# Performance work log

Hardware: AMD Instinct MI355X
Metric: run time of the kernel (lower is better)

Reference implementation:

```python
import jax, jax.numpy as jnp
import numpy as np

N_CIR, N_DIS, D, H = 585, 88, 128, 8
E_CC, E_DD = 20000, 3000
EPS = 1e-16


def _gcn(x, src, dst, ew, W, b, N):
    # PyG GCNConv: add self-loops (weight 1), symmetric normalization, x @ W, scatter-add, + bias
    loop = jnp.arange(N)
    s = jnp.concatenate([src, loop])
    d = jnp.concatenate([dst, loop])
    w = jnp.concatenate([ew, jnp.ones((N,), ew.dtype)])
    deg = jax.ops.segment_sum(w, d, num_segments=N)
    dinv = jnp.where(deg > 0, jax.lax.rsqrt(deg), 0.0)
    norm = dinv[s] * w * dinv[d]                      # [E+N]
    h = x @ W                                         # [N,D]
    out = jax.ops.segment_sum(h[s] * norm[:, None], d, num_segments=N)
    return out + b


def _gat(x, src, dst, ea, W, a_src, a_dst, a_edge, We, b, N):
    # PyG GATConv(heads=H, concat=False, edge_dim=1): self-loops with mean edge_attr fill,
    # leaky_relu attention logits, segment softmax over destination, mean over heads, + bias
    loop = jnp.arange(N)
    s = jnp.concatenate([src, loop])
    d = jnp.concatenate([dst, loop])
    ea = jnp.concatenate([ea, jnp.broadcast_to(ea.mean(0, keepdims=True), (N, ea.shape[1]))], 0)
    h = (x @ W).reshape(N, H, D)                      # [N,H,D]
    e = (ea @ We).reshape(-1, H, D)                   # [E+N,H,D]
    alpha = (h * a_src).sum(-1)[s] + (h * a_dst).sum(-1)[d] + (e * a_edge).sum(-1)
    alpha = jax.nn.leaky_relu(alpha, 0.2)             # [E+N,H]
    amax = jax.ops.segment_max(alpha, d, num_segments=N)
    ex = jnp.exp(alpha - amax[d])
    den = jax.ops.segment_sum(ex, d, num_segments=N)
    alpha = ex / (den[d] + EPS)
    out = jax.ops.segment_sum(h[s] * alpha[:, :, None], d, num_segments=N)  # [N,H,D]
    return out.mean(1) + b


def _branch(x, edges, mat, gw1, gb1, aw, asrc, adst, aedge, awe, ab, gw2, gb2, N):
    src, dst = edges[0], edges[1]
    ew = mat[src, dst]                                # gather edge weights from dense matrix
    f1 = jax.nn.relu(_gcn(x, src, dst, ew, gw1, gb1, N))
    att = jax.nn.relu(_gat(f1, src, dst, ew[:, None], aw, asrc, adst, aedge, awe, ab, N))
    f2 = jax.nn.relu(_gcn(att, src, dst, ew, gw2, gb2, N))
    return f1, f2


def _cnn(f1, f2, Wk, b):
    # Conv2d(2,256,(128,1)) over [1,2,128,N] == per-node GEMM over (2,128) then view/transpose
    Xv = jnp.stack([f1.T, f2.T])                      # [2,D,N]
    return jnp.einsum('ock,ckn->no', Wk[..., 0], Xv) + b  # [N,256]


def setup_inputs():
    ks = jax.random.split(jax.random.key(0), 24)
    rn = lambda i, sh, s=1.0: jax.random.normal(ks[i], sh, jnp.float32) * s
    w = 0.08  # ~glorot scale for fan-in 128
    return {
        'x_cir': rn(0, (N_CIR, D)),
        'x_dis': rn(1, (N_DIS, D)),
        'cc_matrix': jax.random.uniform(ks[2], (N_CIR, N_CIR), jnp.float32),
        'dd_matrix': jax.random.uniform(ks[3], (N_DIS, N_DIS), jnp.float32),
        'gcn_c1_w': rn(4, (D, D), w), 'gcn_c1_b': jnp.zeros((D,), jnp.float32),
        'gat_c_w': rn(5, (D, H * D), w), 'gat_c_asrc': rn(6, (H, D), w),
        'gat_c_adst': rn(7, (H, D), w), 'gat_c_aedge': rn(8, (H, D), w),
        'gat_c_we': rn(9, (1, H * D), w), 'gat_c_b': jnp.zeros((D,), jnp.float32),
        'gcn_c2_w': rn(10, (D, D), w), 'gcn_c2_b': jnp.zeros((D,), jnp.float32),
        'gcn_d1_w': rn(11, (D, D), w), 'gcn_d1_b': jnp.zeros((D,), jnp.float32),
        'gat_d_w': rn(12, (D, H * D), w), 'gat_d_asrc': rn(13, (H, D), w),
        'gat_d_adst': rn(14, (H, D), w), 'gat_d_aedge': rn(15, (H, D), w),
        'gat_d_we': rn(16, (1, H * D), w), 'gat_d_b': jnp.zeros((D,), jnp.float32),
        'gcn_d2_w': rn(17, (D, D), w), 'gcn_d2_b': jnp.zeros((D,), jnp.float32),
        'conv_c_w': rn(18, (256, 2, D, 1), w), 'conv_c_b': jnp.zeros((256,), jnp.float32),
        'conv_d_w': rn(19, (256, 2, D, 1), w), 'conv_d_b': jnp.zeros((256,), jnp.float32),
        'cc_edges': jax.random.randint(ks[20], (2, E_CC), 0, N_CIR),
        'dd_edges': jax.random.randint(ks[21], (2, E_DD), 0, N_DIS),
    }


def reference(x_cir, x_dis, cc_matrix, dd_matrix,
              gcn_c1_w, gcn_c1_b, gat_c_w, gat_c_asrc, gat_c_adst, gat_c_aedge, gat_c_we, gat_c_b,
              gcn_c2_w, gcn_c2_b,
              gcn_d1_w, gcn_d1_b, gat_d_w, gat_d_asrc, gat_d_adst, gat_d_aedge, gat_d_we, gat_d_b,
              gcn_d2_w, gcn_d2_b,
              conv_c_w, conv_c_b, conv_d_w, conv_d_b,
              cc_edges, dd_edges):
    c1, c2 = _branch(x_cir, cc_edges, cc_matrix, gcn_c1_w, gcn_c1_b, gat_c_w, gat_c_asrc,
                     gat_c_adst, gat_c_aedge, gat_c_we, gat_c_b, gcn_c2_w, gcn_c2_b, N_CIR)
    d1, d2 = _branch(x_dis, dd_edges, dd_matrix, gcn_d1_w, gcn_d1_b, gat_d_w, gat_d_asrc,
                     gat_d_adst, gat_d_aedge, gat_d_we, gat_d_b, gcn_d2_w, gcn_d2_b, N_DIS)
    cir_fea = _cnn(c1, c2, conv_c_w, conv_c_b)        # [585,256]
    dis_fea = _cnn(d1, d2, conv_d_w, conv_d_b)        # [88,256]
    return cir_fea @ dis_fea.T, cir_fea, dis_fea
```

## Files before the change

kernel.cpp:

```cpp
#include <hip/hip_runtime.h>

constexpr int NCIR = 585;
constexpr int NDIS = 88;
constexpr int NT   = NCIR + NDIS;
constexpr int DIM  = 128;
constexpr int NH   = 8;
constexpr int ECC  = 20000;
constexpr int EDD  = 3000;
constexpr int ET   = ECC + EDD;
constexpr int CO   = 256;
constexpr int F1C  = (NCIR + 3) / 4;
constexpr int F1D  = (NDIS + 3) / 4;
constexpr int NG   = F1C + F1D;
constexpr int CH   = 64;
constexpr int GBK  = (ET + 255) / 256;
constexpr int GEMB = (NT + 1) / 2;

struct P {
  const float *x_c, *x_d, *mat_c, *mat_d;
  const float *g1w_c, *g1b_c, *aw_c, *as_c, *ad_c, *ae_c, *we_c, *ab_c, *g2w_c, *g2b_c;
  const float *g1w_d, *g1b_d, *aw_d, *as_d, *ad_d, *ae_d, *we_d, *ab_d, *g2w_d, *g2b_d;
  const float *cw_c, *cb_c, *cw_d, *cb_d;
  const int *csrc, *cdst, *dsrc, *ddst;
  float *ew, *dinv, *easum, *wedot, *hs, *hd, *h, *f1, *hg, *fill_w, *psc, *psd, *wdeg;
  int *cnt, *cursor, *rowptr, *fill_s;
  float *out_score, *out_cir, *out_dis;
};

__global__ __launch_bounds__(256) void k_gg(P p){
  __shared__ float r0[256], r1[256];
  int b = blockIdx.x, t = threadIdx.x;
  if (b < GBK){
    int e = b * 256 + t;
    float wc = 0.0f, wdv = 0.0f;
    if (e < ET){
      float w; int d;
      if (e < ECC){
        int s = p.csrc[e]; d = p.cdst[e];
        w = p.mat_c[s * NCIR + d]; wc = w;
      } else {
        int el = e - ECC;
        int s = p.dsrc[el]; d = NCIR + p.ddst[el];
        w = p.mat_d[s * NDIS + (d - NCIR)]; wdv = w;
      }
      p.ew[e] = w;
      atomicAdd(&p.wdeg[d], w);
      atomicAdd(&p.cnt[d], 1);
    }
    r0[t] = wc; r1[t] = wdv;
    __syncthreads();
    for (int st = 128; st; st >>= 1){
      if (t < st){ r0[t] += r0[t + st]; r1[t] += r1[t + st]; }
      __syncthreads();
    }
    if (t == 0){ p.psc[b] = r0[0]; p.psd[b] = r1[0]; }
  } else {
    float* a_sh = r0;
    int ub = (b - GBK) * 2;
    int n = t >> 7, k = t & 127;
    int u = ub + n;
    bool ok = u < NT;
    if (ok){
      int br = u >= NCIR;
      a_sh[n * DIM + k] = br ? p.x_d[(u - NCIR) * DIM + k] : p.x_c[u * DIM + k];
    }
    __syncthreads();
    if (ok){
      const float* W = (u >= NCIR) ? p.g1w_d : p.g1w_c;
      float acc = 0.0f;
      #pragma unroll 8
      for (int c = 0; c < DIM; ++c) acc += a_sh[n * DIM + c] * W[c * DIM + k];
      p.h[u * DIM + k] = acc;
    }
  }
}

__global__ __launch_bounds__(1024) void k_scan(P p){
  __shared__ int sd[1024];
  int t = threadIdx.x;
  int v0 = (t < NT) ? p.cnt[t] : 0;
  sd[t] = v0;
  __syncthreads();
  for (int off = 1; off < 1024; off <<= 1){
    int v = (t >= off) ? sd[t - off] : 0;
    __syncthreads();
    sd[t] += v;
    __syncthreads();
  }
  if (t < NT){
    p.rowptr[t + 1] = sd[t];
    p.cursor[t]     = sd[t] - v0;
    p.dinv[t] = rsqrtf(1.0f + p.wdeg[t]);
  }
  if (t == 0) p.rowptr[0] = 0;
  int wv = t >> 6, lane = t & 63;
  if (wv < 2){
    const float* ps = wv ? p.psd : p.psc;
    float v = ps[lane] + (lane + 64 < GBK ? ps[lane + 64] : 0.0f);
    #pragma unroll
    for (int off = 32; off; off >>= 1) v += __shfl_down(v, off, 64);
    if (lane == 0) p.easum[wv] = v / (wv ? (float)EDD : (float)ECC);
  }
  {
    int hh = wv & 7;
    const float* We = (wv >= 8) ? p.we_d : p.we_c;
    const float* Ae = (wv >= 8) ? p.ae_d : p.ae_c;
    float v = We[hh * DIM + lane] * Ae[hh * DIM + lane]
            + We[hh * DIM + 64 + lane] * Ae[hh * DIM + 64 + lane];
    #pragma unroll
    for (int off = 32; off; off >>= 1) v += __shfl_down(v, off, 64);
    if (lane == 0) p.wedot[wv] = v;
  }
}

__global__ __launch_bounds__(256) void k_fill(P p){
  int e = blockIdx.x * 256 + threadIdx.x;
  if (e >= ET) return;
  int s, d;
  if (e < ECC){ s = p.csrc[e]; d = p.cdst[e]; }
  else { int el = e - ECC; s = NCIR + p.dsrc[el]; d = NCIR + p.ddst[el]; }
  int pos = atomicAdd(&p.cursor[d], 1);
  p.fill_s[pos] = s;
  p.fill_w[pos] = p.ew[e];
}

__global__ __launch_bounds__(128) void k_agg1(P p){
  int d = blockIdx.x, k = threadIdx.x;
  int br = d >= NCIR;
  const float* B1 = br ? p.g1b_d : p.g1b_c;
  float dv = p.dinv[d];
  float acc = B1[k] + p.h[d * DIM + k] * dv * dv;
  int beg = p.rowptr[d], end = p.rowptr[d + 1];
  for (int j = beg; j < end; ++j){
    int s = p.fill_s[j];
    acc += p.h[s * DIM + k] * (p.dinv[s] * p.fill_w[j] * dv);
  }
  p.f1[d * DIM + k] = acc;
}

__global__ __launch_bounds__(256) void k_proj(P p){
  __shared__ float a_sh[4][DIM];
  __shared__ float wred[4][8];
  int b = blockIdx.x, t = threadIdx.x;
  int ng = b >> 2, ct = b & 3;
  int base, count, br;
  if (ng < F1C){ base = ng * 4; count = min(4, NCIR - base); br = 0; }
  else { base = NCIR + (ng - F1C) * 4; count = 4; br = 1; }
  for (int i = 0; i < 2; ++i){
    int idx = t + i * 256, n = idx >> 7, c = idx & 127;
    a_sh[n][c] = (n < count) ? fmaxf(p.f1[(base + n) * DIM + c], 0.0f) : 0.0f;
  }
  __syncthreads();
  const float* W = (br ? p.aw_d : p.aw_c) + ct * 256 + t;
  float acc[4] = {0.f, 0.f, 0.f, 0.f};
  #pragma unroll 4
  for (int c = 0; c < DIM; ++c){
    float w = W[c * 1024];
    acc[0] += a_sh[0][c] * w; acc[1] += a_sh[1][c] * w;
    acc[2] += a_sh[2][c] * w; acc[3] += a_sh[3][c] * w;
  }
  int col = ct * 256 + t;
  for (int n = 0; n < count; ++n)
    p.hg[(size_t)(base + n) * 1024 + col] = acc[n];
  const float* As = br ? p.as_d : p.as_c;
  const float* Ad = br ? p.ad_d : p.ad_c;
  float av = As[col], dw = Ad[col];
  int w = t >> 6;
  #pragma unroll
  for (int n = 0; n < 4; ++n){
    float sdot = acc[n] * av, ddot = acc[n] * dw;
    #pragma unroll
    for (int off = 32; off; off >>= 1){
      sdot += __shfl_down(sdot, off, 64);
      ddot += __shfl_down(ddot, off, 64);
    }
    if ((t & 63) == 0){ wred[w][n * 2] = sdot; wred[w][n * 2 + 1] = ddot; }
  }
  __syncthreads();
  if (t < 16){
    int g = t >> 3, v = t & 7, n = v >> 1, isd = v & 1;
    if (n < count){
      float sum = wred[g * 2][v] + wred[g * 2 + 1][v];
      float* dst = isd ? p.hd : p.hs;
      dst[(base + n) * NH + ct * 2 + g] = sum;
    }
  }
}

__global__ __launch_bounds__(256) void k_att(P p){
  __shared__ float den_sh[NH], hd_sh[NH], inv_sh[NH], wself_sh[NH];
  __shared__ float alpha_sh[CH * NH];
  __shared__ int   s_sh[CH];
  __shared__ float a2[2][DIM];
  __shared__ float attv[DIM];
  __shared__ float part[2][DIM];
  int d = blockIdx.x, t = threadIdx.x;
  int g = t >> 7, k = t & 127;
  int br = d >= NCIR;
  const float* wd = p.wedot + br * NH;
  if (t < NH){ den_sh[t] = 0.0f; hd_sh[t] = p.hd[d * NH + t]; }
  __syncthreads();
  int beg = p.rowptr[d], end = p.rowptr[d + 1];
  int deg = end - beg;
  float slw = p.easum[br];
  for (int idx = t; idx < deg * NH; idx += 256){
    int j = beg + (idx >> 3), hh = idx & 7;
    int s = p.fill_s[j];
    float a = p.hs[s * NH + hh] + hd_sh[hh] + p.fill_w[j] * wd[hh];
    a = a > 0.0f ? a : 0.2f * a;
    atomicAdd(&den_sh[hh], expf(a));
  }
  __syncthreads();
  if (t < NH){
    float a = p.hs[d * NH + t] + hd_sh[t] + slw * wd[t];
    a = a > 0.0f ? a : 0.2f * a;
    float ex = expf(a);
    float inv = 1.0f / (den_sh[t] + ex + 1e-16f) * 0.125f;
    inv_sh[t] = inv;
    wself_sh[t] = ex * inv;
  }
  __syncthreads();
  float acc = 0.0f;
  if (g == 0){
    acc = (br ? p.ab_d : p.ab_c)[k];
    const float* r = p.hg + (size_t)d * 1024;
    #pragma unroll
    for (int hh = 0; hh < NH; ++hh) acc += wself_sh[hh] * r[hh * DIM + k];
  }
  for (int j0 = beg; j0 < end; j0 += CH){
    int m = min(CH, end - j0);
    for (int idx = t; idx < m * NH; idx += 256){
      int jj = idx >> 3, hh = idx & 7;
      int j = j0 + jj;
      int s = p.fill_s[j];
      float a = p.hs[s * NH + hh] + hd_sh[hh] + p.fill_w[j] * wd[hh];
      a = a > 0.0f ? a : 0.2f * a;
      alpha_sh[idx] = expf(a) * inv_sh[hh];
    }
    if (t < m) s_sh[t] = p.fill_s[j0 + t];
    __syncthreads();
    for (int jj = g; jj < m; jj += 2){
      const float* r = p.hg + (size_t)s_sh[jj] * 1024;
      #pragma unroll
      for (int hh = 0; hh < NH; ++hh) acc += alpha_sh[jj * NH + hh] * r[hh * DIM + k];
    }
    __syncthreads();
  }
  a2[g][k] = acc;
  __syncthreads();
  if (g == 0) attv[k] = fmaxf(a2[0][k] + a2[1][k], 0.0f);
  __syncthreads();
  const float* W = br ? p.g2w_d : p.g2w_c;
  float h2 = 0.0f;
  #pragma unroll 8
  for (int c = g * 64; c < g * 64 + 64; ++c) h2 += attv[c] * W[c * DIM + k];
  part[g][k] = h2;
  __syncthreads();
  if (g == 0) p.h[d * DIM + k] = part[0][k] + part[1][k];
}

__global__ __launch_bounds__(256) void k_fuse2(P p){
  __shared__ float s12[4][2 * DIM];
  int b = blockIdx.x, o = threadIdx.x;
  int gbase, count, br; float* out;
  if (b < F1C){ gbase = b * 4; count = min(4, NCIR - gbase); br = 0;
                out = p.out_cir + (size_t)gbase * CO; }
  else { int lb = (b - F1C) * 4; gbase = NCIR + lb; count = 4; br = 1;
         out = p.out_dis + (size_t)lb * CO; }
  const float* B2 = br ? p.g2b_d : p.g2b_c;
  int n2 = o >> 7, k = o & 127;
  for (int r = 0; r < 2; ++r){
    int nn = n2 + r * 2;
    float v1 = 0.0f, v2 = 0.0f;
    if (nn < count){
      int u = gbase + nn;
      float dv = p.dinv[u];
      float acc = B2[k] + p.h[u * DIM + k] * dv * dv;
      int beg = p.rowptr[u], end = p.rowptr[u + 1];
      for (int j = beg; j < end; ++j){
        int s = p.fill_s[j];
        acc += p.h[s * DIM + k] * (p.dinv[s] * p.fill_w[j] * dv);
      }
      v2 = fmaxf(acc, 0.0f);
      v1 = fmaxf(p.f1[u * DIM + k], 0.0f);
    }
    s12[nn][k] = v1;
    s12[nn][DIM + k] = v2;
  }
  __syncthreads();
  const float* W = (br ? p.cw_d : p.cw_c) + o * 2 * DIM;
  float bv = (br ? p.cb_d : p.cb_c)[o];
  float a0 = bv, a1 = bv, a2 = bv, a3 = bv;
  #pragma unroll 4
  for (int q = 0; q < 2 * DIM; ++q){
    float wv = W[q];
    a0 += s12[0][q] * wv; a1 += s12[1][q] * wv;
    a2 += s12[2][q] * wv; a3 += s12[3][q] * wv;
  }
  if (0 < count) out[0 * CO + o] = a0;
  if (1 < count) out[1 * CO + o] = a1;
  if (2 < count) out[2 * CO + o] = a2;
  if (3 < count) out[3 * CO + o] = a3;
}

__global__ void k_final(P p){
  __shared__ float ci[CO];
  int i = blockIdx.x, j = threadIdx.x;
  ci[j]       = p.out_cir[i * CO + j];
  ci[DIM + j] = p.out_cir[i * CO + DIM + j];
  __syncthreads();
  if (j < NDIS){
    const float* dr = p.out_dis + j * CO;
    float acc = 0.0f;
    #pragma unroll 8
    for (int q = 0; q < CO; ++q) acc += ci[q] * dr[q];
    p.out_score[i * NDIS + j] = acc;
  }
}

extern "C" void kernel_launch(void* const* d_in, const int* in_sizes, int n_in,
                              void* d_out, int out_size, void* d_ws, size_t ws_size,
                              hipStream_t stream){
  P p;
  typedef const float* F;
  p.x_c   = (F)d_in[0];  p.x_d   = (F)d_in[1];
  p.mat_c = (F)d_in[2];  p.mat_d = (F)d_in[3];
  p.g1w_c = (F)d_in[4];  p.g1b_c = (F)d_in[5];
  p.aw_c  = (F)d_in[6];  p.as_c  = (F)d_in[7];  p.ad_c = (F)d_in[8];
  p.ae_c  = (F)d_in[9];  p.we_c  = (F)d_in[10]; p.ab_c = (F)d_in[11];
  p.g2w_c = (F)d_in[12]; p.g2b_c = (F)d_in[13];
  p.g1w_d = (F)d_in[14]; p.g1b_d = (F)d_in[15];
  p.aw_d  = (F)d_in[16]; p.as_d  = (F)d_in[17]; p.ad_d = (F)d_in[18];
  p.ae_d  = (F)d_in[19]; p.we_d  = (F)d_in[20]; p.ab_d = (F)d_in[21];
  p.g2w_d = (F)d_in[22]; p.g2b_d = (F)d_in[23];
  p.cw_c  = (F)d_in[24]; p.cb_c  = (F)d_in[25];
  p.cw_d  = (F)d_in[26]; p.cb_d  = (F)d_in[27];
  const int* cc_edges = (const int*)d_in[28];
  const int* dd_edges = (const int*)d_in[29];
  p.csrc = cc_edges;  p.cdst = cc_edges + ECC;
  p.dsrc = dd_edges;  p.ddst = dd_edges + EDD;

  float* out = (float*)d_out;
  p.out_score = out;
  p.out_cir   = out + NCIR * NDIS;
  p.out_dis   = p.out_cir + NCIR * CO;

  float* w = (float*)d_ws;
  auto alloc = [&](size_t n){ float* q = w; w += n; return q; };
  p.ew     = alloc(ET);
  p.wdeg   = alloc(676);
  p.cnt    = (int*)alloc(676);
  p.dinv   = alloc(676);
  p.easum  = alloc(4);
  p.wedot  = alloc(16);
  p.psc    = alloc(92);
  p.psd    = alloc(92);
  p.hs     = alloc((size_t)NT * NH);
  p.hd     = alloc((size_t)NT * NH);
  p.h      = alloc((size_t)NT * DIM);
  p.f1     = alloc((size_t)NT * DIM);
  p.hg     = alloc((size_t)NT * 1024);
  p.fill_w = alloc(ET);
  p.cursor = (int*)alloc(676);
  p.rowptr = (int*)alloc(680);
  p.fill_s = (int*)alloc(ET);

  hipMemsetAsync(p.wdeg, 0, 2 * 676 * sizeof(float), stream);
  k_gg    <<<GBK + GEMB, 256,  0, stream>>>(p);
  k_scan  <<<1,          1024, 0, stream>>>(p);
  k_fill  <<<GBK,        256,  0, stream>>>(p);
  k_agg1  <<<NT,         DIM,  0, stream>>>(p);
  k_proj  <<<NG * 4,     256,  0, stream>>>(p);
  k_att   <<<NT,         256,  0, stream>>>(p);
  k_fuse2 <<<F1C + F1D,  256,  0, stream>>>(p);
  k_final <<<NCIR,       DIM,  0, stream>>>(p);
}
```

Before: 216.5 us.

## Fuse all stages into one cooperative persistent kernel with grid syncs

Replaces the eight separate kernel launches with a single cooperative kernel of 256 blocks that loops over each stage's work items and separates stages with grid-wide barriers. The scan is rewritten to run in one 256-thread block using three chunks with a carry, and the mean edge-weight and edge-dot reductions move to a second block. This targets the launch overhead and inter-kernel gaps of a small, latency-bound pipeline. In exchange, stages with more work items than 256 blocks now serialize per block, the kernel holds the union of all stages' shared memory, and cooperative launch may add its own overhead.

```diff
diff --git a/kernel.cpp b/kernel.cpp
--- a/kernel.cpp
+++ b/kernel.cpp
@@ -1,4 +1,6 @@
 #include <hip/hip_runtime.h>
+#include <hip/hip_cooperative_groups.h>
+namespace cg = cooperative_groups;
 
 constexpr int NCIR = 585;
 constexpr int NDIS = 88;
@@ -15,6 +17,7 @@
 constexpr int CH   = 64;
 constexpr int GBK  = (ET + 255) / 256;
 constexpr int GEMB = (NT + 1) / 2;
+constexpr int GRID = 256;
 
 struct P {
   const float *x_c, *x_d, *mat_c, *mat_d;
@@ -27,301 +30,326 @@
   float *out_score, *out_cir, *out_dis;
 };
 
-__global__ __launch_bounds__(256) void k_gg(P p){
+__global__ __launch_bounds__(256) void k_all(P p){
+  cg::grid_group grid = cg::this_grid();
   __shared__ float r0[256], r1[256];
-  int b = blockIdx.x, t = threadIdx.x;
-  if (b < GBK){
-    int e = b * 256 + t;
-    float wc = 0.0f, wdv = 0.0f;
-    if (e < ET){
-      float w; int d;
-      if (e < ECC){
-        int s = p.csrc[e]; d = p.cdst[e];
-        w = p.mat_c[s * NCIR + d]; wc = w;
-      } else {
-        int el = e - ECC;
-        int s = p.dsrc[el]; d = NCIR + p.ddst[el];
-        w = p.mat_d[s * NDIS + (d - NCIR)]; wdv = w;
-      }
-      p.ew[e] = w;
-      atomicAdd(&p.wdeg[d], w);
-      atomicAdd(&p.cnt[d], 1);
-    }
-    r0[t] = wc; r1[t] = wdv;
-    __syncthreads();
-    for (int st = 128; st; st >>= 1){
-      if (t < st){ r0[t] += r0[t + st]; r1[t] += r1[t + st]; }
-      __syncthreads();
-    }
-    if (t == 0){ p.psc[b] = r0[0]; p.psd[b] = r1[0]; }
-  } else {
-    float* a_sh = r0;
-    int ub = (b - GBK) * 2;
-    int n = t >> 7, k = t & 127;
-    int u = ub + n;
-    bool ok = u < NT;
-    if (ok){
-      int br = u >= NCIR;
-      a_sh[n * DIM + k] = br ? p.x_d[(u - NCIR) * DIM + k] : p.x_c[u * DIM + k];
-    }
-    __syncthreads();
-    if (ok){
-      const float* W = (u >= NCIR) ? p.g1w_d : p.g1w_c;
-      float acc = 0.0f;
-      #pragma unroll 8
-      for (int c = 0; c < DIM; ++c) acc += a_sh[n * DIM + c] * W[c * DIM + k];
-      p.h[u * DIM + k] = acc;
-    }
-  }
-}
-
-__global__ __launch_bounds__(1024) void k_scan(P p){
-  __shared__ int sd[1024];
-  int t = threadIdx.x;
-  int v0 = (t < NT) ? p.cnt[t] : 0;
-  sd[t] = v0;
-  __syncthreads();
-  for (int off = 1; off < 1024; off <<= 1){
-    int v = (t >= off) ? sd[t - off] : 0;
-    __syncthreads();
-    sd[t] += v;
-    __syncthreads();
-  }
-  if (t < NT){
-    p.rowptr[t + 1] = sd[t];
-    p.cursor[t]     = sd[t] - v0;
-    p.dinv[t] = rsqrtf(1.0f + p.wdeg[t]);
-  }
-  if (t == 0) p.rowptr[0] = 0;
-  int wv = t >> 6, lane = t & 63;
-  if (wv < 2){
-    const float* ps = wv ? p.psd : p.psc;
-    float v = ps[lane] + (lane + 64 < GBK ? ps[lane + 64] : 0.0f);
-    #pragma unroll
-    for (int off = 32; off; off >>= 1) v += __shfl_down(v, off, 64);
-    if (lane == 0) p.easum[wv] = v / (wv ? (float)EDD : (float)ECC);
-  }
-  {
-    int hh = wv & 7;
-    const float* We = (wv >= 8) ? p.we_d : p.we_c;
-    const float* Ae = (wv >= 8) ? p.ae_d : p.ae_c;
-    float v = We[hh * DIM + lane] * Ae[hh * DIM + lane]
-            + We[hh * DIM + 64 + lane] * Ae[hh * DIM + 64 + lane];
-    #pragma unroll
-    for (int off = 32; off; off >>= 1) v += __shfl_down(v, off, 64);
-    if (lane == 0) p.wedot[wv] = v;
-  }
-}
-
-__global__ __launch_bounds__(256) void k_fill(P p){
-  int e = blockIdx.x * 256 + threadIdx.x;
-  if (e >= ET) return;
-  int s, d;
-  if (e < ECC){ s = p.csrc[e]; d = p.cdst[e]; }
-  else { int el = e - ECC; s = NCIR + p.dsrc[el]; d = NCIR + p.ddst[el]; }
-  int pos = atomicAdd(&p.cursor[d], 1);
-  p.fill_s[pos] = s;
-  p.fill_w[pos] = p.ew[e];
-}
-
-__global__ __launch_bounds__(128) void k_agg1(P p){
-  int d = blockIdx.x, k = threadIdx.x;
-  int br = d >= NCIR;
-  const float* B1 = br ? p.g1b_d : p.g1b_c;
-  float dv = p.dinv[d];
-  float acc = B1[k] + p.h[d * DIM + k] * dv * dv;
-  int beg = p.rowptr[d], end = p.rowptr[d + 1];
-  for (int j = beg; j < end; ++j){
-    int s = p.fill_s[j];
-    acc += p.h[s * DIM + k] * (p.dinv[s] * p.fill_w[j] * dv);
-  }
-  p.f1[d * DIM + k] = acc;
-}
-
-__global__ __launch_bounds__(256) void k_proj(P p){
-  __shared__ float a_sh[4][DIM];
-  __shared__ float wred[4][8];
-  int b = blockIdx.x, t = threadIdx.x;
-  int ng = b >> 2, ct = b & 3;
-  int base, count, br;
-  if (ng < F1C){ base = ng * 4; count = min(4, NCIR - base); br = 0; }
-  else { base = NCIR + (ng - F1C) * 4; count = 4; br = 1; }
-  for (int i = 0; i < 2; ++i){
-    int idx = t + i * 256, n = idx >> 7, c = idx & 127;
-    a_sh[n][c] = (n < count) ? fmaxf(p.f1[(base + n) * DIM + c], 0.0f) : 0.0f;
-  }
-  __syncthreads();
-  const float* W = (br ? p.aw_d : p.aw_c) + ct * 256 + t;
-  float acc[4] = {0.f, 0.f, 0.f, 0.f};
-  #pragma unroll 4
-  for (int c = 0; c < DIM; ++c){
-    float w = W[c * 1024];
-    acc[0] += a_sh[0][c] * w; acc[1] += a_sh[1][c] * w;
-    acc[2] += a_sh[2][c] * w; acc[3] += a_sh[3][c] * w;
-  }
-  int col = ct * 256 + t;
-  for (int n = 0; n < count; ++n)
-    p.hg[(size_t)(base + n) * 1024 + col] = acc[n];
-  const float* As = br ? p.as_d : p.as_c;
-  const float* Ad = br ? p.ad_d : p.ad_c;
-  float av = As[col], dw = Ad[col];
-  int w = t >> 6;
-  #pragma unroll
-  for (int n = 0; n < 4; ++n){
-    float sdot = acc[n] * av, ddot = acc[n] * dw;
-    #pragma unroll
-    for (int off = 32; off; off >>= 1){
-      sdot += __shfl_down(sdot, off, 64);
-      ddot += __shfl_down(ddot, off, 64);
-    }
-    if ((t & 63) == 0){ wred[w][n * 2] = sdot; wred[w][n * 2 + 1] = ddot; }
-  }
-  __syncthreads();
-  if (t < 16){
-    int g = t >> 3, v = t & 7, n = v >> 1, isd = v & 1;
-    if (n < count){
-      float sum = wred[g * 2][v] + wred[g * 2 + 1][v];
-      float* dst = isd ? p.hd : p.hs;
-      dst[(base + n) * NH + ct * 2 + g] = sum;
-    }
-  }
-}
-
-__global__ __launch_bounds__(256) void k_att(P p){
   __shared__ float den_sh[NH], hd_sh[NH], inv_sh[NH], wself_sh[NH];
   __shared__ float alpha_sh[CH * NH];
   __shared__ int   s_sh[CH];
-  __shared__ float a2[2][DIM];
-  __shared__ float attv[DIM];
-  __shared__ float part[2][DIM];
-  int d = blockIdx.x, t = threadIdx.x;
-  int g = t >> 7, k = t & 127;
-  int br = d >= NCIR;
-  const float* wd = p.wedot + br * NH;
-  if (t < NH){ den_sh[t] = 0.0f; hd_sh[t] = p.hd[d * NH + t]; }
-  __syncthreads();
-  int beg = p.rowptr[d], end = p.rowptr[d + 1];
-  int deg = end - beg;
-  float slw = p.easum[br];
-  for (int idx = t; idx < deg * NH; idx += 256){
-    int j = beg + (idx >> 3), hh = idx & 7;
-    int s = p.fill_s[j];
-    float a = p.hs[s * NH + hh] + hd_sh[hh] + p.fill_w[j] * wd[hh];
-    a = a > 0.0f ? a : 0.2f * a;
-    atomicAdd(&den_sh[hh], expf(a));
-  }
-  __syncthreads();
-  if (t < NH){
-    float a = p.hs[d * NH + t] + hd_sh[t] + slw * wd[t];
-    a = a > 0.0f ? a : 0.2f * a;
-    float ex = expf(a);
-    float inv = 1.0f / (den_sh[t] + ex + 1e-16f) * 0.125f;
-    inv_sh[t] = inv;
-    wself_sh[t] = ex * inv;
-  }
-  __syncthreads();
-  float acc = 0.0f;
-  if (g == 0){
-    acc = (br ? p.ab_d : p.ab_c)[k];
-    const float* r = p.hg + (size_t)d * 1024;
+  __shared__ float attv[DIM], a2[2][DIM], part[2][DIM];
+  __shared__ float a_sh4[4][DIM];
+  __shared__ float wred[4][8];
+  __shared__ float s12[4][2 * DIM];
+  __shared__ int   sc[256];
+  __shared__ int   carry_sh;
+  __shared__ float ci[CO];
+
+  int b = blockIdx.x, t = threadIdx.x;
+
+  for (int u = b; u < GBK + GEMB; u += GRID){
+    if (u < GBK){
+      int e = u * 256 + t;
+      float wc = 0.0f, wdv = 0.0f;
+      if (e < ET){
+        float w; int d;
+        if (e < ECC){
+          int s = p.csrc[e]; d = p.cdst[e];
+          w = p.mat_c[s * NCIR + d]; wc = w;
+        } else {
+          int el = e - ECC;
+          int s = p.dsrc[el]; d = NCIR + p.ddst[el];
+          w = p.mat_d[s * NDIS + (d - NCIR)]; wdv = w;
+        }
+        p.ew[e] = w;
+        atomicAdd(&p.wdeg[d], w);
+        atomicAdd(&p.cnt[d], 1);
+      }
+      r0[t] = wc; r1[t] = wdv;
+      __syncthreads();
+      for (int st = 128; st; st >>= 1){
+        if (t < st){ r0[t] += r0[t + st]; r1[t] += r1[t + st]; }
+        __syncthreads();
+      }
+      if (t == 0){ p.psc[u] = r0[0]; p.psd[u] = r1[0]; }
+      __syncthreads();
+    } else {
+      int ub = (u - GBK) * 2;
+      int n = t >> 7, k = t & 127;
+      int node = ub + n;
+      bool ok = node < NT;
+      if (ok){
+        int br = node >= NCIR;
+        r0[n * DIM + k] = br ? p.x_d[(node - NCIR) * DIM + k] : p.x_c[node * DIM + k];
+      }
+      __syncthreads();
+      if (ok){
+        const float* W = (node >= NCIR) ? p.g1w_d : p.g1w_c;
+        float acc = 0.0f;
+        #pragma unroll 8
+        for (int c = 0; c < DIM; ++c) acc += r0[n * DIM + c] * W[c * DIM + k];
+        p.h[node * DIM + k] = acc;
+      }
+      __syncthreads();
+    }
+  }
+  grid.sync();
+
+  if (b == 0){
+    if (t == 0) carry_sh = 0;
+    __syncthreads();
+    for (int chunk = 0; chunk < 3; ++chunk){
+      int i = chunk * 256 + t;
+      int v = (i < NT) ? p.cnt[i] : 0;
+      sc[t] = v;
+      __syncthreads();
+      for (int off = 1; off < 256; off <<= 1){
+        int tmp = (t >= off) ? sc[t - off] : 0;
+        __syncthreads();
+        sc[t] += tmp;
+        __syncthreads();
+      }
+      int incl = sc[t] + carry_sh;
+      if (i < NT){
+        p.rowptr[i + 1] = incl;
+        p.cursor[i]     = incl - v;
+        p.dinv[i] = rsqrtf(1.0f + p.wdeg[i]);
+      }
+      __syncthreads();
+      if (t == 0) carry_sh += sc[255];
+      __syncthreads();
+    }
+    if (t == 0) p.rowptr[0] = 0;
+  } else if (b == 1){
+    r0[t] = (t < GBK) ? p.psc[t] : 0.0f;
+    r1[t] = (t < GBK) ? p.psd[t] : 0.0f;
+    __syncthreads();
+    for (int st = 128; st; st >>= 1){
+      if (t < st){ r0[t] += r0[t + st]; r1[t] += r1[t + st]; }
+      __syncthreads();
+    }
+    if (t == 0){ p.easum[0] = r0[0] / (float)ECC; p.easum[1] = r1[0] / (float)EDD; }
+    int wv = t >> 6, lane = t & 63;
+    for (int q = 0; q < 4; ++q){
+      int w = wv * 4 + q, hh = w & 7;
+      const float* We = (w >= 8) ? p.we_d : p.we_c;
+      const float* Ae = (w >= 8) ? p.ae_d : p.ae_c;
+      float v = We[hh * DIM + lane] * Ae[hh * DIM + lane]
+              + We[hh * DIM + 64 + lane] * Ae[hh * DIM + 64 + lane];
+      #pragma unroll
+      for (int off = 32; off; off >>= 1) v += __shfl_down(v, off, 64);
+      if (lane == 0) p.wedot[w] = v;
+    }
+  }
+  grid.sync();
+
+  for (int u = b; u < GBK; u += GRID){
+    int e = u * 256 + t;
+    if (e < ET){
+      int s, d;
+      if (e < ECC){ s = p.csrc[e]; d = p.cdst[e]; }
+      else { int el = e - ECC; s = NCIR + p.dsrc[el]; d = NCIR + p.ddst[el]; }
+      int pos = atomicAdd(&p.cursor[d], 1);
+      p.fill_s[pos] = s;
+      p.fill_w[pos] = p.ew[e];
+    }
+  }
+  grid.sync();
+
+  for (int pr = b; pr < GEMB; pr += GRID){
+    int node = pr * 2 + (t >> 7);
+    int k = t & 127;
+    if (node < NT){
+      int br = node >= NCIR;
+      const float* B1 = br ? p.g1b_d : p.g1b_c;
+      float dv = p.dinv[node];
+      float acc = B1[k] + p.h[node * DIM + k] * dv * dv;
+      int beg = p.rowptr[node], end = p.rowptr[node + 1];
+      for (int j = beg; j < end; ++j){
+        int s = p.fill_s[j];
+        acc += p.h[s * DIM + k] * (p.dinv[s] * p.fill_w[j] * dv);
+      }
+      p.f1[node * DIM + k] = acc;
+    }
+  }
+  grid.sync();
+
+  for (int u = b; u < NG * 4; u += GRID){
+    __syncthreads();
+    int ng = u >> 2, ct = u & 3;
+    int base, count, br;
+    if (ng < F1C){ base = ng * 4; count = min(4, NCIR - base); br = 0; }
+    else { base = NCIR + (ng - F1C) * 4; count = 4; br = 1; }
+    for (int i = 0; i < 2; ++i){
+      int idx = t + i * 256, n = idx >> 7, c = idx & 127;
+      a_sh4[n][c] = (n < count) ? fmaxf(p.f1[(base + n) * DIM + c], 0.0f) : 0.0f;
+    }
+    __syncthreads();
+    const float* W = (br ? p.aw_d : p.aw_c) + ct * 256 + t;
+    float acc[4] = {0.f, 0.f, 0.f, 0.f};
+    #pragma unroll 4
+    for (int c = 0; c < DIM; ++c){
+      float w = W[c * 1024];
+      acc[0] += a_sh4[0][c] * w; acc[1] += a_sh4[1][c] * w;
+      acc[2] += a_sh4[2][c] * w; acc[3] += a_sh4[3][c] * w;
+    }
+    int col = ct * 256 + t;
+    for (int n = 0; n < count; ++n)
+      p.hg[(size_t)(base + n) * 1024 + col] = acc[n];
+    const float* As = br ? p.as_d : p.as_c;
+    const float* Ad = br ? p.ad_d : p.ad_c;
+    float av = As[col], dw = Ad[col];
+    int w = t >> 6;
     #pragma unroll
-    for (int hh = 0; hh < NH; ++hh) acc += wself_sh[hh] * r[hh * DIM + k];
-  }
-  for (int j0 = beg; j0 < end; j0 += CH){
-    int m = min(CH, end - j0);
-    for (int idx = t; idx < m * NH; idx += 256){
-      int jj = idx >> 3, hh = idx & 7;
-      int j = j0 + jj;
+    for (int n = 0; n < 4; ++n){
+      float sdot = acc[n] * av, ddot = acc[n] * dw;
+      #pragma unroll
+      for (int off = 32; off; off >>= 1){
+        sdot += __shfl_down(sdot, off, 64);
+        ddot += __shfl_down(ddot, off, 64);
+      }
+      if ((t & 63) == 0){ wred[w][n * 2] = sdot; wred[w][n * 2 + 1] = ddot; }
+    }
+    __syncthreads();
+    if (t < 16){
+      int g = t >> 3, v = t & 7, n = v >> 1, isd = v & 1;
+      if (n < count){
+        float sum = wred[g * 2][v] + wred[g * 2 + 1][v];
+        float* dst = isd ? p.hd : p.hs;
+        dst[(base + n) * NH + ct * 2 + g] = sum;
+      }
+    }
+  }
+  grid.sync();
+
+  for (int d = b; d < NT; d += GRID){
+    __syncthreads();
+    int g = t >> 7, k = t & 127;
+    int br = d >= NCIR;
+    const float* wd = p.wedot + br * NH;
+    if (t < NH){ den_sh[t] = 0.0f; hd_sh[t] = p.hd[d * NH + t]; }
+    __syncthreads();
+    int beg = p.rowptr[d], end = p.rowptr[d + 1];
+    int deg = end - beg;
+    float slw = p.easum[br];
+    for (int idx = t; idx < deg * NH; idx += 256){
+      int j = beg + (idx >> 3), hh = idx & 7;
       int s = p.fill_s[j];
       float a = p.hs[s * NH + hh] + hd_sh[hh] + p.fill_w[j] * wd[hh];
       a = a > 0.0f ? a : 0.2f * a;
-      alpha_sh[idx] = expf(a) * inv_sh[hh];
-    }
-    if (t < m) s_sh[t] = p.fill_s[j0 + t];
-    __syncthreads();
-    for (int jj = g; jj < m; jj += 2){
-      const float* r = p.hg + (size_t)s_sh[jj] * 1024;
+      atomicAdd(&den_sh[hh], expf(a));
+    }
+    __syncthreads();
+    if (t < NH){
+      float a = p.hs[d * NH + t] + hd_sh[t] + slw * wd[t];
+      a = a > 0.0f ? a : 0.2f * a;
+      float ex = expf(a);
+      float inv = 1.0f / (den_sh[t] + ex + 1e-16f) * 0.125f;
+      inv_sh[t] = inv;
+      wself_sh[t] = ex * inv;
+    }
+    __syncthreads();
+    float acc = 0.0f;
+    if (g == 0){
+      acc = (br ? p.ab_d : p.ab_c)[k];
+      const float* r = p.hg + (size_t)d * 1024;
       #pragma unroll
-      for (int hh = 0; hh < NH; ++hh) acc += alpha_sh[jj * NH + hh] * r[hh * DIM + k];
-    }
-    __syncthreads();
-  }
-  a2[g][k] = acc;
-  __syncthreads();
-  if (g == 0) attv[k] = fmaxf(a2[0][k] + a2[1][k], 0.0f);
-  __syncthreads();
-  const float* W = br ? p.g2w_d : p.g2w_c;
-  float h2 = 0.0f;
-  #pragma unroll 8
-  for (int c = g * 64; c < g * 64 + 64; ++c) h2 += attv[c] * W[c * DIM + k];
-  part[g][k] = h2;
-  __syncthreads();
-  if (g == 0) p.h[d * DIM + k] = part[0][k] + part[1][k];
-}
-
-__global__ __launch_bounds__(256) void k_fuse2(P p){
-  __shared__ float s12[4][2 * DIM];
-  int b = blockIdx.x, o = threadIdx.x;
-  int gbase, count, br; float* out;
-  if (b < F1C){ gbase = b * 4; count = min(4, NCIR - gbase); br = 0;
-                out = p.out_cir + (size_t)gbase * CO; }
-  else { int lb = (b - F1C) * 4; gbase = NCIR + lb; count = 4; br = 1;
-         out = p.out_dis + (size_t)lb * CO; }
-  const float* B2 = br ? p.g2b_d : p.g2b_c;
-  int n2 = o >> 7, k = o & 127;
-  for (int r = 0; r < 2; ++r){
-    int nn = n2 + r * 2;
-    float v1 = 0.0f, v2 = 0.0f;
-    if (nn < count){
-      int u = gbase + nn;
-      float dv = p.dinv[u];
-      float acc = B2[k] + p.h[u * DIM + k] * dv * dv;
-      int beg = p.rowptr[u], end = p.rowptr[u + 1];
-      for (int j = beg; j < end; ++j){
+      for (int hh = 0; hh < NH; ++hh) acc += wself_sh[hh] * r[hh * DIM + k];
+    }
+    for (int j0 = beg; j0 < end; j0 += CH){
+      int m = min(CH, end - j0);
+      for (int idx = t; idx < m * NH; idx += 256){
+        int jj = idx >> 3, hh = idx & 7;
+        int j = j0 + jj;
         int s = p.fill_s[j];
-        acc += p.h[s * DIM + k] * (p.dinv[s] * p.fill_w[j] * dv);
-      }
-      v2 = fmaxf(acc, 0.0f);
-      v1 = fmaxf(p.f1[u * DIM + k], 0.0f);
-    }
-    s12[nn][k] = v1;
-    s12[nn][DIM + k] = v2;
-  }
-  __syncthreads();
-  const float* W = (br ? p.cw_d : p.cw_c) + o * 2 * DIM;
-  float bv = (br ? p.cb_d : p.cb_c)[o];
-  float a0 = bv, a1 = bv, a2 = bv, a3 = bv;
-  #pragma unroll 4
-  for (int q = 0; q < 2 * DIM; ++q){
-    float wv = W[q];
-    a0 += s12[0][q] * wv; a1 += s12[1][q] * wv;
-    a2 += s12[2][q] * wv; a3 += s12[3][q] * wv;
-  }
-  if (0 < count) out[0 * CO + o] = a0;
-  if (1 < count) out[1 * CO + o] = a1;
-  if (2 < count) out[2 * CO + o] = a2;
-  if (3 < count) out[3 * CO + o] = a3;
-}
-
-__global__ void k_final(P p){
-  __shared__ float ci[CO];
-  int i = blockIdx.x, j = threadIdx.x;
-  ci[j]       = p.out_cir[i * CO + j];
-  ci[DIM + j] = p.out_cir[i * CO + DIM + j];
-  __syncthreads();
-  if (j < NDIS){
-    const float* dr = p.out_dis + j * CO;
-    float acc = 0.0f;
+        float a = p.hs[s * NH + hh] + hd_sh[hh] + p.fill_w[j] * wd[hh];
+        a = a > 0.0f ? a : 0.2f * a;
+        alpha_sh[idx] = expf(a) * inv_sh[hh];
+      }
+      if (t < m) s_sh[t] = p.fill_s[j0 + t];
+      __syncthreads();
+      for (int jj = g; jj < m; jj += 2){
+        const float* r = p.hg + (size_t)s_sh[jj] * 1024;
+        #pragma unroll
+        for (int hh = 0; hh < NH; ++hh) acc += alpha_sh[jj * NH + hh] * r[hh * DIM + k];
+      }
+      __syncthreads();
+    }
+    a2[g][k] = acc;
+    __syncthreads();
+    if (g == 0) attv[k] = fmaxf(a2[0][k] + a2[1][k], 0.0f);
+    __syncthreads();
+    const float* W = br ? p.g2w_d : p.g2w_c;
+    float h2 = 0.0f;
     #pragma unroll 8
-    for (int q = 0; q < CO; ++q) acc += ci[q] * dr[q];
-    p.out_score[i * NDIS + j] = acc;
+    for (int c = g * 64; c < g * 64 + 64; ++c) h2 += attv[c] * W[c * DIM + k];
+    part[g][k] = h2;
+    __syncthreads();
+    if (g == 0) p.h[d * DIM + k] = part[0][k] + part[1][k];
+  }
+  grid.sync();
+
+  for (int u = b; u < F1C + F1D; u += GRID){
+    __syncthreads();
+    int gbase, count, br; float* out;
+    if (u < F1C){ gbase = u * 4; count = min(4, NCIR - gbase); br = 0;
+                  out = p.out_cir + (size_t)gbase * CO; }
+    else { int lb = (u - F1C) * 4; gbase = NCIR + lb; count = 4; br = 1;
+           out = p.out_dis + (size_t)lb * CO; }
+    const float* B2 = br ? p.g2b_d : p.g2b_c;
+    int n2 = t >> 7, k = t & 127;
+    for (int r = 0; r < 2; ++r){
+      int nn = n2 + r * 2;
+      float v1 = 0.0f, v2 = 0.0f;
+      if (nn < count){
+        int node = gbase + nn;
+        float dv = p.dinv[node];
+        float acc = B2[k] + p.h[node * DIM + k] * dv * dv;
+        int beg = p.rowptr[node], end = p.rowptr[node + 1];
+        for (int j = beg; j < end; ++j){
+          int s = p.fill_s[j];
+          acc += p.h[s * DIM + k] * (p.dinv[s] * p.fill_w[j] * dv);
+        }
+        v2 = fmaxf(acc, 0.0f);
+        v1 = fmaxf(p.f1[node * DIM + k], 0.0f);
+      }
+      s12[nn][k] = v1;
+      s12[nn][DIM + k] = v2;
+    }
+    __syncthreads();
+    const float* W = (br ? p.cw_d : p.cw_c) + t * 2 * DIM;
+    float bv = (br ? p.cb_d : p.cb_c)[t];
+    float c0 = bv, c1 = bv, c2 = bv, c3 = bv;
+    #pragma unroll 4
+    for (int q = 0; q < 2 * DIM; ++q){
+      float wv = W[q];
+      c0 += s12[0][q] * wv; c1 += s12[1][q] * wv;
+      c2 += s12[2][q] * wv; c3 += s12[3][q] * wv;
+    }
+    if (0 < count) out[0 * CO + t] = c0;
+    if (1 < count) out[1 * CO + t] = c1;
+    if (2 < count) out[2 * CO + t] = c2;
+    if (3 < count) out[3 * CO + t] = c3;
+  }
+  grid.sync();
+
+  for (int i = b; i < NCIR; i += GRID){
+    __syncthreads();
+    ci[t] = p.out_cir[i * CO + t];
+    __syncthreads();
+    if (t < NDIS){
+      const float* dr = p.out_dis + t * CO;
+      float acc = 0.0f;
+      #pragma unroll 8
+      for (int q = 0; q < CO; ++q) acc += ci[q] * dr[q];
+      p.out_score[i * NDIS + t] = acc;
+    }
   }
 }
 
 extern "C" void kernel_launch(void* const* d_in, const int* in_sizes, int n_in,
                               void* d_out, int out_size, void* d_ws, size_t ws_size,
                               hipStream_t stream){
-  P p;
+  static P p;
   typedef const float* F;
   p.x_c   = (F)d_in[0];  p.x_d   = (F)d_in[1];
   p.mat_c = (F)d_in[2];  p.mat_d = (F)d_in[3];
@@ -366,12 +394,7 @@
   p.fill_s = (int*)alloc(ET);
 
   hipMemsetAsync(p.wdeg, 0, 2 * 676 * sizeof(float), stream);
-  k_gg    <<<GBK + GEMB, 256,  0, stream>>>(p);
-  k_scan  <<<1,          1024, 0, stream>>>(p);
-  k_fill  <<<GBK,        256,  0, stream>>>(p);
-  k_agg1  <<<NT,         DIM,  0, stream>>>(p);
-  k_proj  <<<NG * 4,     256,  0, stream>>>(p);
-  k_att   <<<NT,         256,  0, stream>>>(p);
-  k_fuse2 <<<F1C + F1D,  256,  0, stream>>>(p);
-  k_final <<<NCIR,       DIM,  0, stream>>>(p);
+  void* args[] = { (void*)&p };
+  hipLaunchCooperativeKernel((const void*)k_all, dim3(GRID), dim3(256),
+                             args, 0, stream);
 }
```

Measured after the change: 489.1 us. 126% more time.

## Replace CSR scan/fill with fixed-capacity per-node buckets and fuse GCN aggregation into projection

Applied to the files above, without the earlier changes.

Edges are now written straight into per-destination buckets of fixed capacity 256 while the degree atomics are taken. This removes the prefix-scan and fill kernels and the rowptr/cursor/dinv/ew buffers. The first GCN aggregation moves into the GAT projection kernel, where each of the four column-tile blocks recomputes it redundantly. The mean edge weight and We·a_edge dot products are now computed per block inside the attention kernel. Kernel launches drop from eight to five, at the cost of extra redundant work, on-the-fly rsqrt of degrees, and silently dropping edges for any node with more than 256 incoming edges.

```diff
diff --git a/kernel.cpp b/kernel.cpp
--- a/kernel.cpp
+++ b/kernel.cpp
@@ -9,6 +9,7 @@
 constexpr int EDD  = 3000;
 constexpr int ET   = ECC + EDD;
 constexpr int CO   = 256;
+constexpr int CAP  = 256;
 constexpr int F1C  = (NCIR + 3) / 4;
 constexpr int F1D  = (NDIS + 3) / 4;
 constexpr int NG   = F1C + F1D;
@@ -22,8 +23,8 @@
   const float *g1w_d, *g1b_d, *aw_d, *as_d, *ad_d, *ae_d, *we_d, *ab_d, *g2w_d, *g2b_d;
   const float *cw_c, *cb_c, *cw_d, *cb_d;
   const int *csrc, *cdst, *dsrc, *ddst;
-  float *ew, *dinv, *easum, *wedot, *hs, *hd, *h, *f1, *hg, *fill_w, *psc, *psd, *wdeg;
-  int *cnt, *cursor, *rowptr, *fill_s;
+  float *hs, *hd, *h, *f1, *hg, *fill_w, *psc, *psd, *wdeg;
+  int *cnt, *fill_s;
   float *out_score, *out_cir, *out_dis;
 };
 
@@ -34,18 +35,21 @@
     int e = b * 256 + t;
     float wc = 0.0f, wdv = 0.0f;
     if (e < ET){
-      float w; int d;
+      float w; int s, d;
       if (e < ECC){
-        int s = p.csrc[e]; d = p.cdst[e];
+        s = p.csrc[e]; d = p.cdst[e];
         w = p.mat_c[s * NCIR + d]; wc = w;
       } else {
         int el = e - ECC;
-        int s = p.dsrc[el]; d = NCIR + p.ddst[el];
-        w = p.mat_d[s * NDIS + (d - NCIR)]; wdv = w;
+        s = NCIR + p.dsrc[el]; d = NCIR + p.ddst[el];
+        w = p.mat_d[(s - NCIR) * NDIS + (d - NCIR)]; wdv = w;
       }
-      p.ew[e] = w;
+      int pos = atomicAdd(&p.cnt[d], 1);
+      if (pos < CAP){
+        p.fill_s[d * CAP + pos] = s;
+        p.fill_w[d * CAP + pos] = w;
+      }
       atomicAdd(&p.wdeg[d], w);
-      atomicAdd(&p.cnt[d], 1);
     }
     r0[t] = wc; r1[t] = wdv;
     __syncthreads();
@@ -55,100 +59,53 @@
     }
     if (t == 0){ p.psc[b] = r0[0]; p.psd[b] = r1[0]; }
   } else {
-    float* a_sh = r0;
     int ub = (b - GBK) * 2;
     int n = t >> 7, k = t & 127;
     int u = ub + n;
     bool ok = u < NT;
     if (ok){
       int br = u >= NCIR;
-      a_sh[n * DIM + k] = br ? p.x_d[(u - NCIR) * DIM + k] : p.x_c[u * DIM + k];
+      r0[n * DIM + k] = br ? p.x_d[(u - NCIR) * DIM + k] : p.x_c[u * DIM + k];
     }
     __syncthreads();
     if (ok){
       const float* W = (u >= NCIR) ? p.g1w_d : p.g1w_c;
       float acc = 0.0f;
       #pragma unroll 8
-      for (int c = 0; c < DIM; ++c) acc += a_sh[n * DIM + c] * W[c * DIM + k];
+      for (int c = 0; c < DIM; ++c) acc += r0[n * DIM + c] * W[c * DIM + k];
       p.h[u * DIM + k] = acc;
     }
   }
 }
 
-__global__ __launch_bounds__(1024) void k_scan(P p){
-  __shared__ int sd[1024];
-  int t = threadIdx.x;
-  int v0 = (t < NT) ? p.cnt[t] : 0;
-  sd[t] = v0;
-  __syncthreads();
-  for (int off = 1; off < 1024; off <<= 1){
-    int v = (t >= off) ? sd[t - off] : 0;
-    __syncthreads();
-    sd[t] += v;
-    __syncthreads();
-  }
-  if (t < NT){
-    p.rowptr[t + 1] = sd[t];
-    p.cursor[t]     = sd[t] - v0;
-    p.dinv[t] = rsqrtf(1.0f + p.wdeg[t]);
-  }
-  if (t == 0) p.rowptr[0] = 0;
-  int wv = t >> 6, lane = t & 63;
-  if (wv < 2){
-    const float* ps = wv ? p.psd : p.psc;
-    float v = ps[lane] + (lane + 64 < GBK ? ps[lane + 64] : 0.0f);
-    #pragma unroll
-    for (int off = 32; off; off >>= 1) v += __shfl_down(v, off, 64);
-    if (lane == 0) p.easum[wv] = v / (wv ? (float)EDD : (float)ECC);
-  }
-  {
-    int hh = wv & 7;
-    const float* We = (wv >= 8) ? p.we_d : p.we_c;
-    const float* Ae = (wv >= 8) ? p.ae_d : p.ae_c;
-    float v = We[hh * DIM + lane] * Ae[hh * DIM + lane]
-            + We[hh * DIM + 64 + lane] * Ae[hh * DIM + 64 + lane];
-    #pragma unroll
-    for (int off = 32; off; off >>= 1) v += __shfl_down(v, off, 64);
-    if (lane == 0) p.wedot[wv] = v;
-  }
-}
-
-__global__ __launch_bounds__(256) void k_fill(P p){
-  int e = blockIdx.x * 256 + threadIdx.x;
-  if (e >= ET) return;
-  int s, d;
-  if (e < ECC){ s = p.csrc[e]; d = p.cdst[e]; }
-  else { int el = e - ECC; s = NCIR + p.dsrc[el]; d = NCIR + p.ddst[el]; }
-  int pos = atomicAdd(&p.cursor[d], 1);
-  p.fill_s[pos] = s;
-  p.fill_w[pos] = p.ew[e];
-}
-
-__global__ __launch_bounds__(128) void k_agg1(P p){
-  int d = blockIdx.x, k = threadIdx.x;
-  int br = d >= NCIR;
-  const float* B1 = br ? p.g1b_d : p.g1b_c;
-  float dv = p.dinv[d];
-  float acc = B1[k] + p.h[d * DIM + k] * dv * dv;
-  int beg = p.rowptr[d], end = p.rowptr[d + 1];
-  for (int j = beg; j < end; ++j){
-    int s = p.fill_s[j];
-    acc += p.h[s * DIM + k] * (p.dinv[s] * p.fill_w[j] * dv);
-  }
-  p.f1[d * DIM + k] = acc;
-}
-
-__global__ __launch_bounds__(256) void k_proj(P p){
-  __shared__ float a_sh[4][DIM];
+__global__ __launch_bounds__(256) void k_aggproj(P p){
+  __shared__ float a_sh4[4][DIM];
   __shared__ float wred[4][8];
   int b = blockIdx.x, t = threadIdx.x;
   int ng = b >> 2, ct = b & 3;
   int base, count, br;
   if (ng < F1C){ base = ng * 4; count = min(4, NCIR - base); br = 0; }
   else { base = NCIR + (ng - F1C) * 4; count = 4; br = 1; }
-  for (int i = 0; i < 2; ++i){
-    int idx = t + i * 256, n = idx >> 7, c = idx & 127;
-    a_sh[n][c] = (n < count) ? fmaxf(p.f1[(base + n) * DIM + c], 0.0f) : 0.0f;
+  const float* B1 = br ? p.g1b_d : p.g1b_c;
+  int n2 = t >> 7, k = t & 127;
+  for (int r = 0; r < 2; ++r){
+    int nn = n2 + r * 2;
+    float v = 0.0f;
+    if (nn < count){
+      int u = base + nn;
+      float dvu = rsqrtf(1.0f + p.wdeg[u]);
+      float acc = B1[k] + p.h[u * DIM + k] * dvu * dvu;
+      int deg = min(p.cnt[u], CAP);
+      const int*   fs = p.fill_s + u * CAP;
+      const float* fw = p.fill_w + u * CAP;
+      for (int j = 0; j < deg; ++j){
+        int s = fs[j];
+        acc += p.h[s * DIM + k] * (rsqrtf(1.0f + p.wdeg[s]) * fw[j] * dvu);
+      }
+      if (ct == 0) p.f1[u * DIM + k] = acc;
+      v = fmaxf(acc, 0.0f);
+    }
+    a_sh4[nn][k] = v;
   }
   __syncthreads();
   const float* W = (br ? p.aw_d : p.aw_c) + ct * 256 + t;
@@ -156,8 +113,8 @@
   #pragma unroll 4
   for (int c = 0; c < DIM; ++c){
     float w = W[c * 1024];
-    acc[0] += a_sh[0][c] * w; acc[1] += a_sh[1][c] * w;
-    acc[2] += a_sh[2][c] * w; acc[3] += a_sh[3][c] * w;
+    acc[0] += a_sh4[0][c] * w; acc[1] += a_sh4[1][c] * w;
+    acc[2] += a_sh4[2][c] * w; acc[3] += a_sh4[3][c] * w;
   }
   int col = ct * 256 + t;
   for (int n = 0; n < count; ++n)
@@ -188,31 +145,50 @@
 }
 
 __global__ __launch_bounds__(256) void k_att(P p){
-  __shared__ float den_sh[NH], hd_sh[NH], inv_sh[NH], wself_sh[NH];
+  __shared__ float den_sh[NH], hd_sh[NH], inv_sh[NH], wself_sh[NH], wd_sh[NH];
+  __shared__ float slw_sh;
   __shared__ float alpha_sh[CH * NH];
   __shared__ int   s_sh[CH];
-  __shared__ float a2[2][DIM];
-  __shared__ float attv[DIM];
-  __shared__ float part[2][DIM];
+  __shared__ float a2[2][DIM], attv[DIM], part[2][DIM];
   int d = blockIdx.x, t = threadIdx.x;
   int g = t >> 7, k = t & 127;
   int br = d >= NCIR;
-  const float* wd = p.wedot + br * NH;
+  int wv = t >> 6, lane = t & 63;
   if (t < NH){ den_sh[t] = 0.0f; hd_sh[t] = p.hd[d * NH + t]; }
-  __syncthreads();
-  int beg = p.rowptr[d], end = p.rowptr[d + 1];
-  int deg = end - beg;
-  float slw = p.easum[br];
+  if (wv == 0){
+    const float* ps = br ? p.psd : p.psc;
+    float v = (lane < GBK ? ps[lane] : 0.0f) + (lane + 64 < GBK ? ps[lane + 64] : 0.0f);
+    #pragma unroll
+    for (int off = 32; off; off >>= 1) v += __shfl_down(v, off, 64);
+    if (lane == 0) slw_sh = v / (br ? (float)EDD : (float)ECC);
+  }
+  if (wv >= 2){
+    const float* We = br ? p.we_d : p.we_c;
+    const float* Ae = br ? p.ae_d : p.ae_c;
+    for (int q = 0; q < 4; ++q){
+      int hh = (wv - 2) * 4 + q;
+      float v = We[hh * DIM + lane] * Ae[hh * DIM + lane]
+              + We[hh * DIM + 64 + lane] * Ae[hh * DIM + 64 + lane];
+      #pragma unroll
+      for (int off = 32; off; off >>= 1) v += __shfl_down(v, off, 64);
+      if (lane == 0) wd_sh[hh] = v;
+    }
+  }
+  __syncthreads();
+  int beg = d * CAP;
+  int deg = min(p.cnt[d], CAP);
+  int end = beg + deg;
+  float slw = slw_sh;
   for (int idx = t; idx < deg * NH; idx += 256){
     int j = beg + (idx >> 3), hh = idx & 7;
     int s = p.fill_s[j];
-    float a = p.hs[s * NH + hh] + hd_sh[hh] + p.fill_w[j] * wd[hh];
+    float a = p.hs[s * NH + hh] + hd_sh[hh] + p.fill_w[j] * wd_sh[hh];
     a = a > 0.0f ? a : 0.2f * a;
     atomicAdd(&den_sh[hh], expf(a));
   }
   __syncthreads();
   if (t < NH){
-    float a = p.hs[d * NH + t] + hd_sh[t] + slw * wd[t];
+    float a = p.hs[d * NH + t] + hd_sh[t] + slw * wd_sh[t];
     a = a > 0.0f ? a : 0.2f * a;
     float ex = expf(a);
     float inv = 1.0f / (den_sh[t] + ex + 1e-16f) * 0.125f;
@@ -233,7 +209,7 @@
       int jj = idx >> 3, hh = idx & 7;
       int j = j0 + jj;
       int s = p.fill_s[j];
-      float a = p.hs[s * NH + hh] + hd_sh[hh] + p.fill_w[j] * wd[hh];
+      float a = p.hs[s * NH + hh] + hd_sh[hh] + p.fill_w[j] * wd_sh[hh];
       a = a > 0.0f ? a : 0.2f * a;
       alpha_sh[idx] = expf(a) * inv_sh[hh];
     }
@@ -274,12 +250,14 @@
     float v1 = 0.0f, v2 = 0.0f;
     if (nn < count){
       int u = gbase + nn;
-      float dv = p.dinv[u];
-      float acc = B2[k] + p.h[u * DIM + k] * dv * dv;
-      int beg = p.rowptr[u], end = p.rowptr[u + 1];
-      for (int j = beg; j < end; ++j){
-        int s = p.fill_s[j];
-        acc += p.h[s * DIM + k] * (p.dinv[s] * p.fill_w[j] * dv);
+      float dvu = rsqrtf(1.0f + p.wdeg[u]);
+      float acc = B2[k] + p.h[u * DIM + k] * dvu * dvu;
+      int deg = min(p.cnt[u], CAP);
+      const int*   fs = p.fill_s + u * CAP;
+      const float* fw = p.fill_w + u * CAP;
+      for (int j = 0; j < deg; ++j){
+        int s = fs[j];
+        acc += p.h[s * DIM + k] * (rsqrtf(1.0f + p.wdeg[s]) * fw[j] * dvu);
       }
       v2 = fmaxf(acc, 0.0f);
       v1 = fmaxf(p.f1[u * DIM + k], 0.0f);
@@ -347,12 +325,8 @@
 
   float* w = (float*)d_ws;
   auto alloc = [&](size_t n){ float* q = w; w += n; return q; };
-  p.ew     = alloc(ET);
   p.wdeg   = alloc(676);
   p.cnt    = (int*)alloc(676);
-  p.dinv   = alloc(676);
-  p.easum  = alloc(4);
-  p.wedot  = alloc(16);
   p.psc    = alloc(92);
   p.psd    = alloc(92);
   p.hs     = alloc((size_t)NT * NH);
@@ -360,18 +334,13 @@
   p.h      = alloc((size_t)NT * DIM);
   p.f1     = alloc((size_t)NT * DIM);
   p.hg     = alloc((size_t)NT * 1024);
-  p.fill_w = alloc(ET);
-  p.cursor = (int*)alloc(676);
-  p.rowptr = (int*)alloc(680);
-  p.fill_s = (int*)alloc(ET);
+  p.fill_w = alloc((size_t)NT * CAP);
+  p.fill_s = (int*)alloc((size_t)NT * CAP);
 
   hipMemsetAsync(p.wdeg, 0, 2 * 676 * sizeof(float), stream);
-  k_gg    <<<GBK + GEMB, 256,  0, stream>>>(p);
-  k_scan  <<<1,          1024, 0, stream>>>(p);
-  k_fill  <<<GBK,        256,  0, stream>>>(p);
-  k_agg1  <<<NT,         DIM,  0, stream>>>(p);
-  k_proj  <<<NG * 4,     256,  0, stream>>>(p);
-  k_att   <<<NT,         256,  0, stream>>>(p);
-  k_fuse2 <<<F1C + F1D,  256,  0, stream>>>(p);
-  k_final <<<NCIR,       DIM,  0, stream>>>(p);
-}
+  k_gg     <<<GBK + GEMB, 256, 0, stream>>>(p);
+  k_aggproj<<<NG * 4,     256, 0, stream>>>(p);
+  k_att    <<<NT,         256, 0, stream>>>(p);
+  k_fuse2  <<<F1C + F1D,  256, 0, stream>>>(p);
+  k_final  <<<NCIR,       DIM, 0, stream>>>(p);
+}
```

New measurement: 222.0 us. 1.03x slower.
